# Performance work log

Hardware: AMD Instinct MI355X
Metric: run time of the kernel (lower is better)

Reference implementation:

```python
import jax, jax.numpy as jnp
import numpy as np
import itertools


def _build_tables():
    y_table = np.array([[16, 11, 10, 16, 24, 40, 51, 61], [12, 12, 14, 19, 26, 58, 60, 55],
                        [14, 13, 16, 24, 40, 57, 69, 56], [14, 17, 22, 29, 51, 87, 80, 62],
                        [18, 22, 37, 56, 68, 109, 103, 77], [24, 35, 55, 64, 81, 104, 113, 92],
                        [49, 64, 78, 87, 103, 121, 120, 101], [72, 92, 95, 98, 112, 100, 103, 99]],
                       dtype=np.float32).T
    c_table = np.full((8, 8), 99, dtype=np.float32)
    c_table[:4, :4] = np.array([[17, 18, 24, 47], [18, 21, 26, 66], [24, 26, 56, 99], [47, 66, 99, 99]],
                               dtype=np.float32).T
    a = np.array([1.0 / np.sqrt(2)] + [1.0] * 7, dtype=np.float32)
    alpha = np.outer(a, a).astype(np.float32)
    idct_t = np.zeros((8, 8, 8, 8), dtype=np.float32)
    for x, y, u, v in itertools.product(range(8), repeat=4):
        idct_t[x, y, u, v] = np.cos((2 * u + 1) * x * np.pi / 16) * np.cos((2 * v + 1) * y * np.pi / 16)
    matrix = np.array([[1.0, 0.0, 1.402], [1.0, -0.344136, -0.714136], [1.0, 1.772, 0.0]],
                      dtype=np.float32).T
    shift = np.array([0.0, -128.0, -128.0], dtype=np.float32)
    return y_table, c_table, alpha, idct_t, matrix, shift


def setup_inputs() -> dict:
    key = jax.random.key(0)
    k1, k2, k3 = jax.random.split(key, 3)
    B, H, W = 16, 1024, 1024
    y = jax.random.normal(k1, (B, (H * W) // 64, 8, 8), dtype=jnp.float32)
    cb = jax.random.normal(k2, (B, (H // 2) * (W // 2) // 64, 8, 8), dtype=jnp.float32)
    cr = jax.random.normal(k3, (B, (H // 2) * (W // 2) // 64, 8, 8), dtype=jnp.float32)
    y_table, c_table, alpha, idct_t, matrix, shift = _build_tables()
    return {"y": y, "cb": cb, "cr": cr, "height": H, "width": W, "factor": 1,
            "y_table": jnp.asarray(y_table), "c_table": jnp.asarray(c_table),
            "alpha": jnp.asarray(alpha), "idct_tensor": jnp.asarray(idct_t),
            "matrix": jnp.asarray(matrix), "shift": jnp.asarray(shift)}


def _idct_8x8(blocks, alpha, idct_tensor):
    # blocks: [B, N, 8, 8] dequantized coefficients
    x = blocks * alpha  # broadcast over last two dims
    return 0.25 * jnp.einsum('bnuv,uvxy->bnxy', x, idct_tensor) + 128.0


def _merge(patches, h, w):
    # [B, h*w/64, 8, 8] -> [B, h, w]
    B = patches.shape[0]
    x = patches.reshape(B, h // 8, w // 8, 8, 8)
    return x.transpose(0, 1, 3, 2, 4).reshape(B, h, w)


def _upsample2(x):
    return jnp.repeat(jnp.repeat(x, 2, axis=1), 2, axis=2)


def reference(y, cb, cr, height, width, factor, y_table, c_table, alpha, idct_tensor, matrix, shift):
    f = jnp.float32(factor)
    y_img = _merge(_idct_8x8(y * (y_table * f), alpha, idct_tensor), height, width)
    cb_img = _merge(_idct_8x8(cb * (c_table * f), alpha, idct_tensor), height // 2, width // 2)
    cr_img = _merge(_idct_8x8(cr * (c_table * f), alpha, idct_tensor), height // 2, width // 2)
    ycbcr = jnp.stack([y_img, _upsample2(cb_img), _upsample2(cr_img)], axis=-1)  # [B,H,W,3]
    rgb = jnp.einsum('bhwc,cd->bhwd', ycbcr + shift, matrix)
    rgb = rgb.transpose(0, 3, 1, 2)  # [B,3,H,W]
    return jnp.clip(rgb, 0.0, 255.0) / 255.0
```

## Files before the change

kernel.cpp:

```cpp
#include <hip/hip_runtime.h>
#include <hip/hip_bf16.h>
#include <stdint.h>


__device__ __forceinline__ float read_scalar_as_float(const void* p) {
    unsigned bits = *(const unsigned*)p;
    unsigned e = (bits >> 23) & 0xffu;
    if (e >= 64u && e <= 191u) return __uint_as_float(bits);
    return (float)(int)bits;
}

__global__ __launch_bounds__(256) void jpeg_decode_kernel(
    const float* __restrict__ gy,
    const float* __restrict__ gcb,
    const float* __restrict__ gcr,
    const void* __restrict__ p_h,
    const void* __restrict__ p_w,
    const void* __restrict__ p_f,
    const float* __restrict__ y_table,
    const float* __restrict__ c_table,
    const float* __restrict__ alpha,
    const float* __restrict__ idct_t,
    const float* __restrict__ cmat,
    const float* __restrict__ shift,
    float* __restrict__ out,
    int y_size)
{
    __shared__ float sCoef[768];
    __shared__ float sTmp[768];
    __shared__ float sM[64];
    __shared__ float sY[512];
    __shared__ float sCb[128];
    __shared__ float sCr[128];

    const int H = (int)read_scalar_as_float(p_h);
    const int W = (int)read_scalar_as_float(p_w);
    const float f = read_scalar_as_float(p_f);

    const int HW = H * W;
    const int B = y_size / HW;
    const int tiles_x = W >> 5;
    const int tiles_y = H >> 4;
    const int tiles_per_img = tiles_x * tiles_y;
    const int n_tiles = B * tiles_per_img;

    const int tid = threadIdx.x;

    for (int tile = blockIdx.x; tile < n_tiles; tile += gridDim.x) {
        const int b  = tile / tiles_per_img;
        const int r  = tile - b * tiles_per_img;
        const int ty = r / tiles_x;
        const int tx = r - ty * tiles_x;

        if (tid < 64) {
            sM[tid] = idct_t[(tid >> 3) * 512 + (tid & 7) * 8];
        }
        const int wb = W >> 3;
        #pragma unroll
        for (int i = 0; i < 3; ++i) {
            const int t   = tid + i * 256;
            const int blk = t >> 6;
            const int p   = t & 63;
            float v;
            if (blk < 8) {
                const int by = blk >> 2, bx = blk & 3;
                const int n  = (ty * 2 + by) * wb + (tx * 4 + bx);
                v = gy[((size_t)b * (HW >> 6) + n) * 64 + p]
                    * (y_table[p] * f) * alpha[p];
            } else {
                const int k = (blk - 8) & 1;
                const int n = ty * (W >> 4) + tx * 2 + k;
                const float* src = (blk < 10) ? gcb : gcr;
                v = src[((size_t)b * (HW >> 8) + n) * 64 + p]
                    * (c_table[p] * f) * alpha[p];
            }
            sCoef[t] = v;
        }
        __syncthreads();

        #pragma unroll
        for (int i = 0; i < 3; ++i) {
            const int t  = tid + i * 256;
            const int yy = t & 7;
            const int cbase = t & ~7;
            float acc = 0.f;
            #pragma unroll
            for (int v = 0; v < 8; ++v)
                acc += sCoef[cbase + v] * sM[v * 8 + yy];
            sTmp[t] = acc;
        }
        __syncthreads();

        #pragma unroll
        for (int i = 0; i < 3; ++i) {
            const int t   = tid + i * 256;
            const int blk = t >> 6;
            const int p   = t & 63;
            const int x   = p >> 3;
            const int yy  = p & 7;
            const int tbase = (t & ~63);
            float acc = 0.f;
            #pragma unroll
            for (int u = 0; u < 8; ++u)
                acc += sM[u * 8 + x] * sTmp[tbase + u * 8 + yy];
            const float val = 0.25f * acc + 128.0f;
            if (blk < 8) {
                const int by = blk >> 2, bx = blk & 3;
                sY[(by * 8 + x) * 32 + bx * 8 + yy] = val;
            } else if (blk < 10) {
                sCb[x * 16 + (blk - 8) * 8 + yy] = val;
            } else {
                sCr[x * 16 + (blk - 10) * 8 + yy] = val;
            }
        }

        const float m00 = cmat[0], m01 = cmat[1], m02 = cmat[2];
        const float m10 = cmat[3], m11 = cmat[4], m12 = cmat[5];
        const float m20 = cmat[6], m21 = cmat[7], m22 = cmat[8];
        const float s0 = shift[0], s1 = shift[1], s2 = shift[2];
        __syncthreads();

        const size_t obase = (size_t)b * 3 * HW;
        const int row0 = ty * 16;
        const int col0 = tx * 32;
        #pragma unroll
        for (int i = 0; i < 2; ++i) {
            const int q  = tid + i * 256;
            const int py = q >> 5;
            const int px = q & 31;
            const float yv = sY[py * 32 + px] + s0;
            const int ci = (py >> 1) * 16 + (px >> 1);
            const float cbv = sCb[ci] + s1;
            const float crv = sCr[ci] + s2;
            float rr = yv * m00 + cbv * m10 + crv * m20;
            float gg = yv * m01 + cbv * m11 + crv * m21;
            float bb = yv * m02 + cbv * m12 + crv * m22;
            rr = fminf(fmaxf(rr, 0.f), 255.f) * (1.0f / 255.0f);
            gg = fminf(fmaxf(gg, 0.f), 255.f) * (1.0f / 255.0f);
            bb = fminf(fmaxf(bb, 0.f), 255.f) * (1.0f / 255.0f);
            const size_t pix = (size_t)(row0 + py) * W + (col0 + px);
            out[obase + pix]            = rr;
            out[obase + (size_t)HW + pix]   = gg;
            out[obase + 2 * (size_t)HW + pix] = bb;
        }
        __syncthreads();
    }
}

extern "C" void kernel_launch(void* const* d_in, const int* in_sizes, int n_in,
                              void* d_out, int out_size, void* d_ws, size_t ws_size,
                              hipStream_t stream) {
    const float* gy   = (const float*)d_in[0];
    const float* gcb  = (const float*)d_in[1];
    const float* gcr  = (const float*)d_in[2];
    const void*  p_h  = d_in[3];
    const void*  p_w  = d_in[4];
    const void*  p_f  = d_in[5];
    const float* y_t  = (const float*)d_in[6];
    const float* c_t  = (const float*)d_in[7];
    const float* al   = (const float*)d_in[8];
    const float* idct = (const float*)d_in[9];
    const float* mat  = (const float*)d_in[10];
    const float* shf  = (const float*)d_in[11];
    float* out = (float*)d_out;

    int n_tiles = out_size / 1536;
    if (n_tiles < 1) n_tiles = 1;

    jpeg_decode_kernel<<<dim3(n_tiles), dim3(256), 0, stream>>>(
        gy, gcb, gcr, p_h, p_w, p_f, y_t, c_t, al, idct, mat, shf,
        out, in_sizes[0]);
}
```

Baseline: 330.4 us.

## Use 32x32 tiles with float4 loads/stores and precomputed dequant-IDCT tables

Each block now covers a 32x32 pixel tile: 16 Y blocks plus 4 Cb and 4 Cr blocks. Global loads and output stores use float4 vectors. The quantization and alpha scaling is folded into per-thread IDCT coefficients, and the tables are loaded once per block outside the tile loop. Shared buffers are padded to reduce bank conflicts. The grid is halved, so each block carries more work and more shared memory, which could lower occupancy.

```diff
diff --git a/kernel.cpp b/kernel.cpp
--- a/kernel.cpp
+++ b/kernel.cpp
@@ -26,12 +26,14 @@
     float* __restrict__ out,
     int y_size)
 {
-    __shared__ float sCoef[768];
-    __shared__ float sTmp[768];
+    __shared__ float sQY[64];
+    __shared__ float sQC[64];
     __shared__ float sM[64];
-    __shared__ float sY[512];
-    __shared__ float sCb[128];
-    __shared__ float sCr[128];
+    __shared__ float sCoef[1536];
+    __shared__ float sTmp[1536];
+    __shared__ float sY[32 * 36];
+    __shared__ float sCb[16 * 20];
+    __shared__ float sCr[16 * 20];
 
     const int H = (int)read_scalar_as_float(p_h);
     const int W = (int)read_scalar_as_float(p_w);
@@ -40,108 +42,137 @@
     const int HW = H * W;
     const int B = y_size / HW;
     const int tiles_x = W >> 5;
-    const int tiles_y = H >> 4;
-    const int tiles_per_img = tiles_x * tiles_y;
-    const int n_tiles = B * tiles_per_img;
+    const int tiles_y = H >> 5;
+    const int tpi = tiles_x * tiles_y;
+    const int n_tiles = B * tpi;
 
     const int tid = threadIdx.x;
 
+    if (tid < 64) {
+        const float a = alpha[tid];
+        sQY[tid] = y_table[tid] * f * a;
+        sQC[tid] = c_table[tid] * f * a;
+        sM[tid]  = idct_t[(tid >> 3) * 512 + (tid & 7) * 8];
+    }
+    const float m00 = cmat[0], m01 = cmat[1], m02 = cmat[2];
+    const float m10 = cmat[3], m11 = cmat[4], m12 = cmat[5];
+    const float m20 = cmat[6], m21 = cmat[7], m22 = cmat[8];
+    const float s0 = shift[0], s1 = shift[1], s2 = shift[2];
+    __syncthreads();
+
     for (int tile = blockIdx.x; tile < n_tiles; tile += gridDim.x) {
-        const int b  = tile / tiles_per_img;
-        const int r  = tile - b * tiles_per_img;
+        const int b  = tile / tpi;
+        const int r  = tile - b * tpi;
         const int ty = r / tiles_x;
         const int tx = r - ty * tiles_x;
 
-        if (tid < 64) {
-            sM[tid] = idct_t[(tid >> 3) * 512 + (tid & 7) * 8];
-        }
-        const int wb = W >> 3;
-        #pragma unroll
-        for (int i = 0; i < 3; ++i) {
-            const int t   = tid + i * 256;
-            const int blk = t >> 6;
-            const int p   = t & 63;
-            float v;
-            if (blk < 8) {
-                const int by = blk >> 2, bx = blk & 3;
-                const int n  = (ty * 2 + by) * wb + (tx * 4 + bx);
-                v = gy[((size_t)b * (HW >> 6) + n) * 64 + p]
-                    * (y_table[p] * f) * alpha[p];
-            } else {
-                const int k = (blk - 8) & 1;
-                const int n = ty * (W >> 4) + tx * 2 + k;
-                const float* src = (blk < 10) ? gcb : gcr;
-                v = src[((size_t)b * (HW >> 8) + n) * 64 + p]
-                    * (c_table[p] * f) * alpha[p];
-            }
-            sCoef[t] = v;
-        }
-        __syncthreads();
-
-        #pragma unroll
-        for (int i = 0; i < 3; ++i) {
-            const int t  = tid + i * 256;
-            const int yy = t & 7;
-            const int cbase = t & ~7;
-            float acc = 0.f;
-            #pragma unroll
-            for (int v = 0; v < 8; ++v)
-                acc += sCoef[cbase + v] * sM[v * 8 + yy];
-            sTmp[t] = acc;
-        }
-        __syncthreads();
-
-        #pragma unroll
-        for (int i = 0; i < 3; ++i) {
-            const int t   = tid + i * 256;
-            const int blk = t >> 6;
-            const int p   = t & 63;
-            const int x   = p >> 3;
-            const int yy  = p & 7;
-            const int tbase = (t & ~63);
-            float acc = 0.f;
-            #pragma unroll
-            for (int u = 0; u < 8; ++u)
-                acc += sM[u * 8 + x] * sTmp[tbase + u * 8 + yy];
-            const float val = 0.25f * acc + 128.0f;
-            if (blk < 8) {
-                const int by = blk >> 2, bx = blk & 3;
-                sY[(by * 8 + x) * 32 + bx * 8 + yy] = val;
-            } else if (blk < 10) {
-                sCb[x * 16 + (blk - 8) * 8 + yy] = val;
-            } else {
-                sCr[x * 16 + (blk - 10) * 8 + yy] = val;
-            }
-        }
-
-        const float m00 = cmat[0], m01 = cmat[1], m02 = cmat[2];
-        const float m10 = cmat[3], m11 = cmat[4], m12 = cmat[5];
-        const float m20 = cmat[6], m21 = cmat[7], m22 = cmat[8];
-        const float s0 = shift[0], s1 = shift[1], s2 = shift[2];
-        __syncthreads();
-
-        const size_t obase = (size_t)b * 3 * HW;
-        const int row0 = ty * 16;
-        const int col0 = tx * 32;
-        #pragma unroll
-        for (int i = 0; i < 2; ++i) {
-            const int q  = tid + i * 256;
-            const int py = q >> 5;
-            const int px = q & 31;
-            const float yv = sY[py * 32 + px] + s0;
-            const int ci = (py >> 1) * 16 + (px >> 1);
-            const float cbv = sCb[ci] + s1;
-            const float crv = sCr[ci] + s2;
-            float rr = yv * m00 + cbv * m10 + crv * m20;
-            float gg = yv * m01 + cbv * m11 + crv * m21;
-            float bb = yv * m02 + cbv * m12 + crv * m22;
-            rr = fminf(fmaxf(rr, 0.f), 255.f) * (1.0f / 255.0f);
-            gg = fminf(fmaxf(gg, 0.f), 255.f) * (1.0f / 255.0f);
-            bb = fminf(fmaxf(bb, 0.f), 255.f) * (1.0f / 255.0f);
-            const size_t pix = (size_t)(row0 + py) * W + (col0 + px);
-            out[obase + pix]            = rr;
-            out[obase + (size_t)HW + pix]   = gg;
-            out[obase + 2 * (size_t)HW + pix] = bb;
+        {
+            const int blk = tid >> 4;
+            const int p4  = (tid & 15) * 4;
+            const int by = blk >> 2, bx = blk & 3;
+            const int n  = (ty * 4 + by) * (W >> 3) + tx * 4 + bx;
+            const float4 v = *(const float4*)(gy + ((size_t)b * (HW >> 6) + n) * 64 + p4);
+            *(float4*)(sCoef + blk * 64 + p4) = v;
+            if (tid < 128) {
+                const int cblk = tid >> 4;
+                const int cp4  = (tid & 15) * 4;
+                const int c  = cblk & 3;
+                const int cy = c >> 1, cx = c & 1;
+                const int cn = (ty * 2 + cy) * (W >> 4) + tx * 2 + cx;
+                const float* src = (cblk < 4) ? gcb : gcr;
+                const float4 cv = *(const float4*)(src + ((size_t)b * (HW >> 8) + cn) * 64 + cp4);
+                *(float4*)(sCoef + 1024 + cblk * 64 + cp4) = cv;
+            }
+        }
+        __syncthreads();
+
+        {
+            const int p  = tid & 63;
+            const int u  = p >> 3;
+            const int yy = p & 7;
+            float pmy[8], pmc[8];
+            #pragma unroll
+            for (int v = 0; v < 8; ++v) {
+                const float mv = sM[v * 8 + yy];
+                pmy[v] = sQY[u * 8 + v] * mv;
+                pmc[v] = sQC[u * 8 + v] * mv;
+            }
+            const int blk0 = tid >> 6;
+            #pragma unroll
+            for (int i = 0; i < 6; ++i) {
+                const int blk = blk0 + i * 4;
+                const float4 c0 = *(const float4*)(sCoef + blk * 64 + u * 8);
+                const float4 c1 = *(const float4*)(sCoef + blk * 64 + u * 8 + 4);
+                const float* pm = (i < 4) ? pmy : pmc;
+                float acc = c0.x * pm[0] + c0.y * pm[1] + c0.z * pm[2] + c0.w * pm[3]
+                          + c1.x * pm[4] + c1.y * pm[5] + c1.z * pm[6] + c1.w * pm[7];
+                sTmp[blk * 64 + yy * 8 + u] = acc;
+            }
+        }
+        __syncthreads();
+
+        {
+            const int p  = tid & 63;
+            const int x  = p >> 3;
+            const int yy = p & 7;
+            float mu[8];
+            #pragma unroll
+            for (int u = 0; u < 8; ++u) mu[u] = sM[u * 8 + x];
+            const int blk0 = tid >> 6;
+            #pragma unroll
+            for (int i = 0; i < 6; ++i) {
+                const int blk = blk0 + i * 4;
+                const float4 t0 = *(const float4*)(sTmp + blk * 64 + yy * 8);
+                const float4 t1 = *(const float4*)(sTmp + blk * 64 + yy * 8 + 4);
+                float acc = t0.x * mu[0] + t0.y * mu[1] + t0.z * mu[2] + t0.w * mu[3]
+                          + t1.x * mu[4] + t1.y * mu[5] + t1.z * mu[6] + t1.w * mu[7];
+                const float val = 0.25f * acc + 128.0f;
+                if (i < 4) {
+                    const int by = blk >> 2, bx = blk & 3;
+                    sY[(by * 8 + x) * 36 + bx * 8 + yy] = val;
+                } else if (i == 4) {
+                    const int c = blk - 16;
+                    sCb[((c >> 1) * 8 + x) * 20 + (c & 1) * 8 + yy] = val;
+                } else {
+                    const int c = blk - 20;
+                    sCr[((c >> 1) * 8 + x) * 20 + (c & 1) * 8 + yy] = val;
+                }
+            }
+        }
+        __syncthreads();
+
+        {
+            const int py  = tid >> 3;
+            const int px  = (tid & 7) * 4;
+            const float4 yv4 = *(const float4*)(sY + py * 36 + px);
+            const int crow = (py >> 1) * 20;
+            const int ccol = px >> 1;
+            const float cb0 = sCb[crow + ccol]     + s1;
+            const float cb1 = sCb[crow + ccol + 1] + s1;
+            const float cr0 = sCr[crow + ccol]     + s2;
+            const float cr1 = sCr[crow + ccol + 1] + s2;
+
+            float yv[4] = { yv4.x + s0, yv4.y + s0, yv4.z + s0, yv4.w + s0 };
+            float cbv[4] = { cb0, cb0, cb1, cb1 };
+            float crv[4] = { cr0, cr0, cr1, cr1 };
+
+            float4 Rv, Gv, Bv;
+            float* rp = &Rv.x; float* gp = &Gv.x; float* bp = &Bv.x;
+            #pragma unroll
+            for (int j = 0; j < 4; ++j) {
+                float rr = yv[j] * m00 + cbv[j] * m10 + crv[j] * m20;
+                float gg = yv[j] * m01 + cbv[j] * m11 + crv[j] * m21;
+                float bb = yv[j] * m02 + cbv[j] * m12 + crv[j] * m22;
+                rp[j] = fminf(fmaxf(rr, 0.f), 255.f) * (1.0f / 255.0f);
+                gp[j] = fminf(fmaxf(gg, 0.f), 255.f) * (1.0f / 255.0f);
+                bp[j] = fminf(fmaxf(bb, 0.f), 255.f) * (1.0f / 255.0f);
+            }
+
+            const size_t obase = (size_t)b * 3 * HW;
+            const size_t pix = (size_t)(ty * 32 + py) * W + (tx * 32 + px);
+            *(float4*)(out + obase + pix)                    = Rv;
+            *(float4*)(out + obase + (size_t)HW + pix)       = Gv;
+            *(float4*)(out + obase + 2 * (size_t)HW + pix)   = Bv;
         }
         __syncthreads();
     }
@@ -164,7 +195,7 @@
     const float* shf  = (const float*)d_in[11];
     float* out = (float*)d_out;
 
-    int n_tiles = out_size / 1536;
+    int n_tiles = out_size / 3072;
     if (n_tiles < 1) n_tiles = 1;
 
     jpeg_decode_kernel<<<dim3(n_tiles), dim3(256), 0, stream>>>(
```

New measurement: 293.9 us. 11.1% less time.
